# Optimization experiments

Measured on AMD Instinct MI355X. Metric: run time of the kernel, lower is better.

## Reference

```python
import jax, jax.numpy as jnp
import numpy as np

NEG_SLOPE = 0.2
EPS = 1e-16  # PyG softmax eps


def _gat_conv(x, src, dst, W, att_src, att_dst, bias, heads, out_ch):
    """PyG GATConv (eval mode, self-loops already appended, concat output)."""
    N = x.shape[0]
    xw = (x @ W).reshape(N, heads, out_ch)            # [N,H,C]
    a_src = jnp.sum(xw * att_src, axis=-1)            # [N,H]
    a_dst = jnp.sum(xw * att_dst, axis=-1)            # [N,H]
    e = jax.nn.leaky_relu(a_src[src] + a_dst[dst], NEG_SLOPE)  # [E,H]
    m = jax.ops.segment_max(e, dst, num_segments=N)   # [N,H] (self-loops -> no empty segs)
    e = jnp.exp(e - m[dst])
    denom = jax.ops.segment_sum(e, dst, num_segments=N)
    alpha = e / (denom[dst] + EPS)                    # [E,H]
    msg = xw[src] * alpha[:, :, None]                 # [E,H,C]
    out = jax.ops.segment_sum(msg, dst, num_segments=N)  # [N,H,C]
    return out.reshape(N, heads * out_ch) + bias


def setup_inputs() -> dict:
    key = jax.random.key(0)
    ks = jax.random.split(key, 12)
    N, E, F_in, H, C, NC = 20000, 320000, 512, 8, 64, 32
    x = jax.random.normal(ks[0], (N, F_in), dtype=jnp.float32)
    edge_index = jax.random.randint(ks[1], (2, E), 0, N, dtype=jnp.int64)
    g = lambda k, shape, fan: jax.random.normal(k, shape, dtype=jnp.float32) * (1.0 / np.sqrt(fan))
    return {
        "x": x,
        "edge_index": edge_index,
        "W1": g(ks[2], (F_in, H * C), F_in),
        "att_src1": g(ks[3], (H, C), C),
        "att_dst1": g(ks[4], (H, C), C),
        "b1": jnp.zeros((H * C,), dtype=jnp.float32),
        "W2": g(ks[5], (H * C, NC), H * C),
        "att_src2": g(ks[6], (1, NC), NC),
        "att_dst2": g(ks[7], (1, NC), NC),
        "b2": jnp.zeros((NC,), dtype=jnp.float32),
    }


def reference(x, edge_index, W1, att_src1, att_dst1, b1, W2, att_src2, att_dst2, b2):
    N = x.shape[0]
    H, C = att_src1.shape
    NC = att_src2.shape[1]
    # GATConv adds self-loops by default
    loops = jnp.arange(N, dtype=edge_index.dtype)
    src = jnp.concatenate([edge_index[0], loops])
    dst = jnp.concatenate([edge_index[1], loops])
    h = _gat_conv(x, src, dst, W1, att_src1, att_dst1, b1, H, C)
    h = jax.nn.elu(h)
    h = _gat_conv(h, src, dst, W2, att_src2, att_dst2, b2, 1, NC)
    return jax.nn.log_softmax(h, axis=1)
```

## Files before the change

kernel.cpp:

```cpp
#include <hip/hip_runtime.h>
#include <math.h>

#define NEG_SLOPE 0.2f
#define SM_EPS 1e-16f

typedef short short8 __attribute__((ext_vector_type(8)));
typedef float floatx4 __attribute__((ext_vector_type(4)));


__device__ inline unsigned short f2bf(float x) {
    unsigned int u = __float_as_uint(x);
    unsigned int r = (u + 0x7FFFu + ((u >> 16) & 1u)) >> 16;
    return (unsigned short)r;
}

__device__ inline float bf2f(unsigned short h) {
    return __uint_as_float(((unsigned int)h) << 16);
}

__device__ inline float bflo(unsigned int u) { return __uint_as_float(u << 16); }
__device__ inline float bfhi(unsigned int u) { return __uint_as_float(u & 0xFFFF0000u); }

__device__ __forceinline__ void gl_lds16(const unsigned short* g, unsigned short* l) {
    __builtin_amdgcn_global_load_lds(
        (const __attribute__((address_space(1))) unsigned int*)(g),
        (__attribute__((address_space(3))) unsigned int*)(l), 16, 0, 0);
}

__device__ inline void get_edge(const int* __restrict__ srcA, const int* __restrict__ dstA,
                                int e, int E, int& s, int& d) {
    if (e < E) { s = srcA[e]; d = dstA[e]; }
    else { s = e - E; d = e - E; }
}


__global__ __launch_bounds__(256) void k_prep(const float* __restrict__ x,
                                              unsigned short* __restrict__ xb,
                                              const float* __restrict__ W1,
                                              unsigned short* __restrict__ w1t,
                                              const float* __restrict__ W2,
                                              unsigned short* __restrict__ w2bt,
                                              const int* __restrict__ dstA,
                                              int E, int Ep,
                                              int* __restrict__ deg,
                                              int nblk_deg, int nblk_x) {
    __shared__ float tile[32][33];
    int bx = blockIdx.x;
    int t = threadIdx.x;
    if (bx < nblk_deg) {
        int e = bx * 256 + t;
        if (e < Ep) {
            int d = (e < E) ? dstA[e] : (e - E);
            atomicAdd(&deg[d], 1);
        }
    } else if (bx < nblk_deg + nblk_x) {
        int i = ((bx - nblk_deg) * 256 + t) * 4;
        float4 v = *(const float4*)(x + i);
        ushort4 o;
        o.x = f2bf(v.x); o.y = f2bf(v.y); o.z = f2bf(v.z); o.w = f2bf(v.w);
        *(ushort4*)(xb + i) = o;
    } else if (bx < nblk_deg + nblk_x + 256) {
        int b = bx - nblk_deg - nblk_x;
        int kb = (b & 15) * 32;
        int nb = (b >> 4) * 32;
        int tx = t & 31, ty = t >> 5;
        #pragma unroll
        for (int i = 0; i < 32; i += 8)
            tile[ty + i][tx] = W1[(size_t)(kb + ty + i) * 512 + nb + tx];
        __syncthreads();
        #pragma unroll
        for (int i = 0; i < 32; i += 8)
            w1t[(size_t)(nb + ty + i) * 512 + kb + tx] = f2bf(tile[tx][ty + i]);
    } else {
        int i = (bx - nblk_deg - nblk_x - 256) * 256 + t;
        int c = i >> 9, k = i & 511;
        w2bt[i] = f2bf(W2[k * 32 + c]);
    }
}


__global__ __launch_bounds__(256) void k_scan1(const int* __restrict__ deg, int* __restrict__ incl,
                                               int* __restrict__ part, int N) {
    __shared__ int sm[256];
    int t = threadIdx.x;
    int i = blockIdx.x * 256 + t;
    int v = (i < N) ? deg[i] : 0;
    sm[t] = v; __syncthreads();
    for (int o = 1; o < 256; o <<= 1) {
        int x = (t >= o) ? sm[t - o] : 0;
        __syncthreads();
        sm[t] += x;
        __syncthreads();
    }
    if (i < N) incl[i] = sm[t];
    if (t == 255) part[blockIdx.x] = sm[255];
}

__global__ __launch_bounds__(256) void k_scan3(const int* __restrict__ incl, const int* __restrict__ part,
                                               const int* __restrict__ deg, int* __restrict__ off,
                                               int* __restrict__ cursor, int N) {
    __shared__ int sm[256];
    int bx = blockIdx.x, t = threadIdx.x;
    int partial = 0;
    for (int i = t; i < bx; i += 256) partial += part[i];
    sm[t] = partial; __syncthreads();
    for (int o = 128; o > 0; o >>= 1) {
        if (t < o) sm[t] += sm[t + o];
        __syncthreads();
    }
    int base = sm[0];
    int i = bx * 256 + t;
    if (i >= N) return;
    int v = incl[i] + base;
    off[i + 1] = v;
    cursor[i] = v - deg[i];
    if (i == 0) off[0] = 0;
}

__global__ __launch_bounds__(256) void k_scatter(const int* __restrict__ srcA, const int* __restrict__ dstA,
                                                 int E, int Ep, int* __restrict__ cursor,
                                                 int* __restrict__ src_s) {
    int e = blockIdx.x * 256 + threadIdx.x;
    if (e >= Ep) return;
    int s, d; get_edge(srcA, dstA, e, E, s, d);
    int p = atomicAdd(&cursor[d], 1);
    src_s[p] = s;
}


__global__ __launch_bounds__(256) void k_gemm1_mfma(const unsigned short* __restrict__ A,
                                                    const unsigned short* __restrict__ Bt,
                                                    const float* __restrict__ att_s,
                                                    const float* __restrict__ att_d,
                                                    unsigned short* __restrict__ C,
                                                    float* __restrict__ a_sd,
                                                    float* __restrict__ a_dd, int M) {
    const int K = 512;
    __shared__ unsigned short As[128 * 32];
    __shared__ unsigned short Bs[128 * 32];
    int t = threadIdx.x;
    int lane = t & 63;
    int w = t >> 6;
    int row0 = blockIdx.x * 128;
    int col0 = blockIdx.y * 128;
    int wm = (w >> 1) * 64, wn = (w & 1) * 64;
    int l15 = lane & 15, q = lane >> 4;

    int mrow = t >> 2;
    int kk = (t & 3) * 8;
    unsigned short* ldsA0 = &As[w * 512];
    unsigned short* ldsA1 = &As[2048 + w * 512];
    unsigned short* ldsB0 = &Bs[w * 512];
    unsigned short* ldsB1 = &Bs[2048 + w * 512];

    floatx4 acc[4][4] = {};

    for (int k0 = 0; k0 < K; k0 += 32) {
        gl_lds16(A  + (size_t)(row0 + mrow) * K + k0 + kk,      ldsA0);
        gl_lds16(A  + (size_t)(row0 + 64 + mrow) * K + k0 + kk, ldsA1);
        gl_lds16(Bt + (size_t)(col0 + mrow) * K + k0 + kk,      ldsB0);
        gl_lds16(Bt + (size_t)(col0 + 64 + mrow) * K + k0 + kk, ldsB1);
        __syncthreads();
        short8 af[4], bfr[4];
        #pragma unroll
        for (int i = 0; i < 4; ++i)
            af[i] = *(const short8*)(&As[(wm + i * 16 + l15) * 32 + q * 8]);
        #pragma unroll
        for (int j = 0; j < 4; ++j)
            bfr[j] = *(const short8*)(&Bs[(wn + j * 16 + l15) * 32 + q * 8]);
        #pragma unroll
        for (int i = 0; i < 4; ++i)
            #pragma unroll
            for (int j = 0; j < 4; ++j)
                acc[i][j] = __builtin_amdgcn_mfma_f32_16x16x32_bf16(af[i], bfr[j], acc[i][j], 0, 0, 0);
        __syncthreads();
    }

    #pragma unroll
    for (int i = 0; i < 4; ++i) {
        #pragma unroll
        for (int p = 0; p < 4; ++p) {
            int r = row0 + wm + i * 16 + q * 4 + p;
            if (r < M) {
                #pragma unroll
                for (int j = 0; j < 4; ++j) {
                    int c = col0 + wn + j * 16 + l15;
                    C[(size_t)r * 512 + c] = f2bf(acc[i][j][p]);
                }
            }
        }
    }

    int hh = blockIdx.y * 2 + (w & 1);
    float asr[4], adr[4];
    #pragma unroll
    for (int j = 0; j < 4; ++j) {
        asr[j] = att_s[hh * 64 + j * 16 + l15];
        adr[j] = att_d[hh * 64 + j * 16 + l15];
    }
    #pragma unroll
    for (int i = 0; i < 4; ++i) {
        #pragma unroll
        for (int p = 0; p < 4; ++p) {
            float ds = 0.f, dd = 0.f;
            #pragma unroll
            for (int j = 0; j < 4; ++j) {
                ds = fmaf(acc[i][j][p], asr[j], ds);
                dd = fmaf(acc[i][j][p], adr[j], dd);
            }
            #pragma unroll
            for (int mk = 1; mk <= 8; mk <<= 1) {
                ds += __shfl_xor(ds, mk);
                dd += __shfl_xor(dd, mk);
            }
            int r = row0 + wm + i * 16 + q * 4 + p;
            if (l15 == 0 && r < M) {
                a_sd[(size_t)hh * M + r] = ds;
                a_dd[(size_t)hh * M + r] = dd;
            }
        }
    }
}


__global__ __launch_bounds__(256) void k_l1(const unsigned short* __restrict__ xw,
                                            const float* __restrict__ a_s,
                                            const float* __restrict__ a_d,
                                            const int* __restrict__ off,
                                            const int* __restrict__ src_s,
                                            const float* __restrict__ bias,
                                            unsigned short* __restrict__ hout, int N) {
    int wid = threadIdx.x >> 6, lane = threadIdx.x & 63;
    int h = blockIdx.x & 7;
    int n = (blockIdx.x >> 3) * 32 + wid * 8 + (lane >> 3);
    int li = lane & 7;
    if (n >= N) return;
    int p0 = off[n], p1 = off[n + 1];
    const float* ash = a_s + (size_t)h * N;
    float adv = a_d[(size_t)h * N + n];
    const size_t cbase = (size_t)h * 64 + (size_t)li * 8;

    float acc[8] = {};
    float s = 0.f;
    int p = p0;
    for (; p + 2 <= p1; p += 2) {
        int s0 = src_s[p];
        int s1 = src_s[p + 1];
        const uint4 u0 = *(const uint4*)(xw + (size_t)s0 * 512 + cbase);
        const uint4 u1 = *(const uint4*)(xw + (size_t)s1 * 512 + cbase);
        float e0 = ash[s0] + adv; e0 = e0 > 0.f ? e0 : NEG_SLOPE * e0;
        float e1 = ash[s1] + adv; e1 = e1 > 0.f ? e1 : NEG_SLOPE * e1;
        float w0 = __expf(e0);
        float w1 = __expf(e1);
        s += w0 + w1;
        acc[0] = fmaf(w0, bflo(u0.x), acc[0]); acc[1] = fmaf(w0, bfhi(u0.x), acc[1]);
        acc[2] = fmaf(w0, bflo(u0.y), acc[2]); acc[3] = fmaf(w0, bfhi(u0.y), acc[3]);
        acc[4] = fmaf(w0, bflo(u0.z), acc[4]); acc[5] = fmaf(w0, bfhi(u0.z), acc[5]);
        acc[6] = fmaf(w0, bflo(u0.w), acc[6]); acc[7] = fmaf(w0, bfhi(u0.w), acc[7]);
        acc[0] = fmaf(w1, bflo(u1.x), acc[0]); acc[1] = fmaf(w1, bfhi(u1.x), acc[1]);
        acc[2] = fmaf(w1, bflo(u1.y), acc[2]); acc[3] = fmaf(w1, bfhi(u1.y), acc[3]);
        acc[4] = fmaf(w1, bflo(u1.z), acc[4]); acc[5] = fmaf(w1, bfhi(u1.z), acc[5]);
        acc[6] = fmaf(w1, bflo(u1.w), acc[6]); acc[7] = fmaf(w1, bfhi(u1.w), acc[7]);
    }
    if (p < p1) {
        int s0 = src_s[p];
        const uint4 u0 = *(const uint4*)(xw + (size_t)s0 * 512 + cbase);
        float e0 = ash[s0] + adv; e0 = e0 > 0.f ? e0 : NEG_SLOPE * e0;
        float w0 = __expf(e0);
        s += w0;
        acc[0] = fmaf(w0, bflo(u0.x), acc[0]); acc[1] = fmaf(w0, bfhi(u0.x), acc[1]);
        acc[2] = fmaf(w0, bflo(u0.y), acc[2]); acc[3] = fmaf(w0, bfhi(u0.y), acc[3]);
        acc[4] = fmaf(w0, bflo(u0.z), acc[4]); acc[5] = fmaf(w0, bfhi(u0.z), acc[5]);
        acc[6] = fmaf(w0, bflo(u0.w), acc[6]); acc[7] = fmaf(w0, bfhi(u0.w), acc[7]);
    }

    float inv = 1.f / (s + SM_EPS);
    unsigned int ov[4];
    #pragma unroll
    for (int j = 0; j < 4; ++j) {
        float v0 = acc[2 * j] * inv     + bias[cbase + 2 * j];
        float v1 = acc[2 * j + 1] * inv + bias[cbase + 2 * j + 1];
        v0 = v0 > 0.f ? v0 : expm1f(v0);
        v1 = v1 > 0.f ? v1 : expm1f(v1);
        ov[j] = (unsigned int)f2bf(v0) | ((unsigned int)f2bf(v1) << 16);
    }
    *(uint4*)(hout + (size_t)n * 512 + cbase) = make_uint4(ov[0], ov[1], ov[2], ov[3]);
}


__global__ __launch_bounds__(256) void k_gemm2_mfma(const unsigned short* __restrict__ A,
                                                    const unsigned short* __restrict__ Bt,
                                                    const float* __restrict__ att_s,
                                                    const float* __restrict__ att_d,
                                                    unsigned short* __restrict__ O,
                                                    float* __restrict__ a_s, float* __restrict__ a_d,
                                                    int M) {
    const int K = 512;
    __shared__ unsigned short As[64 * 40];
    __shared__ unsigned short Bs[32 * 40];
    int t = threadIdx.x;
    int lane = t & 63;
    int w = t >> 6;
    int row0 = blockIdx.x * 64;
    int l15 = lane & 15, q = lane >> 4;

    floatx4 acc[2] = {};

    for (int k0 = 0; k0 < K; k0 += 32) {
        {
            int flat = t * 8;
            int m = flat >> 5, kk = flat & 31;
            uint4 va = make_uint4(0u, 0u, 0u, 0u);
            int gr = row0 + m;
            if (gr < M) va = *(const uint4*)(A + (size_t)gr * K + k0 + kk);
            *(uint4*)(&As[m * 40 + kk]) = va;
            if (t < 128) {
                int nn = t >> 2, kb = (t & 3) * 8;
                *(uint4*)(&Bs[nn * 40 + kb]) = *(const uint4*)(Bt + (size_t)nn * K + k0 + kb);
            }
        }
        __syncthreads();
        short8 af = *(const short8*)(&As[(w * 16 + l15) * 40 + q * 8]);
        short8 b0 = *(const short8*)(&Bs[(l15) * 40 + q * 8]);
        short8 b1 = *(const short8*)(&Bs[(16 + l15) * 40 + q * 8]);
        acc[0] = __builtin_amdgcn_mfma_f32_16x16x32_bf16(af, b0, acc[0], 0, 0, 0);
        acc[1] = __builtin_amdgcn_mfma_f32_16x16x32_bf16(af, b1, acc[1], 0, 0, 0);
        __syncthreads();
    }

    float as_lo = att_s[l15], as_hi = att_s[16 + l15];
    float ad_lo = att_d[l15], ad_hi = att_d[16 + l15];
    #pragma unroll
    for (int p = 0; p < 4; ++p) {
        int r = row0 + w * 16 + q * 4 + p;
        bool ok = r < M;
        float v0 = acc[0][p], v1 = acc[1][p];
        if (ok) {
            O[(size_t)r * 32 + l15]      = f2bf(v0);
            O[(size_t)r * 32 + 16 + l15] = f2bf(v1);
        }
        float ds = v0 * as_lo + v1 * as_hi;
        float dd = v0 * ad_lo + v1 * ad_hi;
        #pragma unroll
        for (int mk = 1; mk <= 8; mk <<= 1) {
            ds += __shfl_xor(ds, mk);
            dd += __shfl_xor(dd, mk);
        }
        if (ok && l15 == 0) { a_s[r] = ds; a_d[r] = dd; }
    }
}


__global__ __launch_bounds__(256) void k_l2(const unsigned short* __restrict__ hw2,
                                            const float* __restrict__ a_s,
                                            const float* __restrict__ a_d,
                                            const int* __restrict__ off,
                                            const int* __restrict__ src_s,
                                            const float* __restrict__ bias,
                                            float* __restrict__ outp, int N) {
    int wid = threadIdx.x >> 6, lane = threadIdx.x & 63;
    int n = blockIdx.x * 4 + wid;
    if (n >= N) return;
    int p0 = off[n], p1 = off[n + 1];
    float adv = a_d[n];
    int c = lane & 31, ep = lane >> 5;

    float acc = 0.f, s = 0.f;
    int p = p0;
    for (; p + 64 <= p1; p += 64) {
        int bsrc = src_s[p + lane];
        float e = a_s[bsrc] + adv;
        e = e > 0.f ? e : NEG_SLOPE * e;
        float w64 = __expf(e);
        #pragma unroll
        for (int j = 0; j < 64; j += 2) {
            int sj = __shfl(bsrc, j + ep);
            float wj = __shfl(w64, j + ep);
            s += wj;
            acc = fmaf(wj, bf2f(hw2[(size_t)sj * 32 + c]), acc);
        }
    }
    if (p < p1) {
        int nb = p1 - p;
        int bsrc = src_s[p + (lane < nb ? lane : 0)];
        float e = a_s[bsrc] + adv;
        e = e > 0.f ? e : NEG_SLOPE * e;
        float w64 = __expf(e);
        for (int j = 0; j < nb; j += 2) {
            int idx = j + ep;
            bool valid = idx < nb;
            int idc = valid ? idx : 0;
            int sj = __shfl(bsrc, idc);
            float wj = __shfl(w64, idc);
            if (valid) {
                s += wj;
                acc = fmaf(wj, bf2f(hw2[(size_t)sj * 32 + c]), acc);
            }
        }
    }
    acc += __shfl_xor(acc, 32);
    s   += __shfl_xor(s, 32);
    float v = acc / (s + SM_EPS) + bias[c];
    float mx = v;
    #pragma unroll
    for (int mk = 16; mk >= 1; mk >>= 1) mx = fmaxf(mx, __shfl_xor(mx, mk, 32));
    float ex = __expf(v - mx);
    float sum = ex;
    #pragma unroll
    for (int mk = 16; mk >= 1; mk >>= 1) sum += __shfl_xor(sum, mk, 32);
    if (lane < 32) outp[(size_t)n * 32 + c] = (v - mx) - __logf(sum);
}


extern "C" void kernel_launch(void* const* d_in, const int* in_sizes, int n_in,
                              void* d_out, int out_size, void* d_ws, size_t ws_size,
                              hipStream_t stream) {
    const float* x   = (const float*)d_in[0];
    const int*   ei  = (const int*)d_in[1];
    const float* W1  = (const float*)d_in[2];
    const float* as1 = (const float*)d_in[3];
    const float* ad1 = (const float*)d_in[4];
    const float* b1  = (const float*)d_in[5];
    const float* W2  = (const float*)d_in[6];
    const float* as2 = (const float*)d_in[7];
    const float* ad2 = (const float*)d_in[8];
    const float* b2  = (const float*)d_in[9];
    float* out = (float*)d_out;

    const int F = 512;
    const int N = in_sizes[0] / F;
    const int E = in_sizes[1] / 2;
    const int Ep = E + N;
    const int* srcA = ei;
    const int* dstA = ei + E;

    char* w = (char*)d_ws;
    auto alloc = [&](size_t b) -> void* {
        void* p = (void*)w;
        w += (b + 255) & ~(size_t)255;
        return p;
    };
    unsigned short* xbf  = (unsigned short*)alloc((size_t)N * 512 * 2);
    unsigned short* w1t  = (unsigned short*)alloc((size_t)512 * 512 * 2);
    unsigned short* w2bt = (unsigned short*)alloc((size_t)32 * 512 * 2);
    unsigned short* xw1  = (unsigned short*)alloc((size_t)N * 512 * 2);
    unsigned short* hbuf = (unsigned short*)alloc((size_t)N * 512 * 2);
    float* a_s1 = (float*)alloc((size_t)N * 8 * 4);
    float* a_d1 = (float*)alloc((size_t)N * 8 * 4);
    unsigned short* hw2 = (unsigned short*)alloc((size_t)N * 32 * 2);
    float* a_s2 = (float*)alloc((size_t)N * 4);
    float* a_d2 = (float*)alloc((size_t)N * 4);
    int* deg    = (int*)alloc((size_t)N * 4);
    int* incl   = (int*)alloc((size_t)N * 4);
    int* part   = (int*)alloc(256 * 4);
    int* off    = (int*)alloc((size_t)(N + 1) * 4);
    int* cursor = (int*)alloc((size_t)N * 4);
    int* src_s  = (int*)alloc((size_t)Ep * 4);

    int egrid = (Ep + 255) / 256;
    int sgrid = (N + 255) / 256;
    int ngrid4 = (N + 3) / 4;
    int nblk_x = (N * 512 / 4) / 256;
    int nblk_w2 = (32 * 512 + 255) / 256;

    hipMemsetAsync(deg, 0, (size_t)N * 4, stream);

    k_prep<<<egrid + nblk_x + 256 + nblk_w2, 256, 0, stream>>>(
        x, xbf, W1, w1t, W2, w2bt, dstA, E, Ep, deg, egrid, nblk_x);

    k_scan1<<<sgrid, 256, 0, stream>>>(deg, incl, part, N);
    k_scan3<<<sgrid, 256, 0, stream>>>(incl, part, deg, off, cursor, N);
    k_scatter<<<egrid, 256, 0, stream>>>(srcA, dstA, E, Ep, cursor, src_s);

    {
        dim3 g1((N + 127) / 128, 512 / 128);
        k_gemm1_mfma<<<g1, 256, 0, stream>>>(xbf, w1t, as1, ad1, xw1, a_s1, a_d1, N);
    }
    {
        int ngrid32 = (N + 31) / 32;
        k_l1<<<ngrid32 * 8, 256, 0, stream>>>(xw1, a_s1, a_d1, off, src_s, b1, hbuf, N);
    }

    k_gemm2_mfma<<<(N + 63) / 64, 256, 0, stream>>>(hbuf, w2bt, as2, ad2, hw2, a_s2, a_d2, N);
    k_l2<<<ngrid4, 256, 0, stream>>>(hw2, a_s2, a_d2, off, src_s, b2, out, N);
}
```

Baseline: 250.9 us.

## Sort nodes by degree bins to balance layer-1 aggregation work

Adds a 64-bin degree histogram during the scan, a bin prefix scan, and a permutation pass fused into the scatter kernel, so that the layer-1 aggregation kernel processes nodes grouped by similar in-degree. This is meant to cut divergence among the 8 nodes sharing a wavefront, whose loops run for different edge counts. It also swaps expm1f for __expf-1 in the ELU. The cost is an extra tiny kernel launch, global atomics on 64 bins, and output writes to permuted node rows, which scatters store locality.

```diff
diff --git a/kernel.cpp b/kernel.cpp
--- a/kernel.cpp
+++ b/kernel.cpp
@@ -80,12 +80,16 @@
 
 
 __global__ __launch_bounds__(256) void k_scan1(const int* __restrict__ deg, int* __restrict__ incl,
-                                               int* __restrict__ part, int N) {
+                                               int* __restrict__ part, int* __restrict__ bins, int N) {
     __shared__ int sm[256];
+    __shared__ int hist[64];
     int t = threadIdx.x;
+    if (t < 64) hist[t] = 0;
     int i = blockIdx.x * 256 + t;
     int v = (i < N) ? deg[i] : 0;
-    sm[t] = v; __syncthreads();
+    sm[t] = v;
+    __syncthreads();
+    if (i < N) atomicAdd(&hist[v < 63 ? v : 63], 1);
     for (int o = 1; o < 256; o <<= 1) {
         int x = (t >= o) ? sm[t - o] : 0;
         __syncthreads();
@@ -94,6 +98,15 @@
     }
     if (i < N) incl[i] = sm[t];
     if (t == 255) part[blockIdx.x] = sm[255];
+    __syncthreads();
+    if (t < 64 && hist[t]) atomicAdd(&bins[t], hist[t]);
+}
+
+__global__ void k_binscan(const int* __restrict__ bins, int* __restrict__ bincur) {
+    if (threadIdx.x == 0) {
+        int run = 0;
+        for (int i = 0; i < 64; ++i) { bincur[i] = run; run += bins[i]; }
+    }
 }
 
 __global__ __launch_bounds__(256) void k_scan3(const int* __restrict__ incl, const int* __restrict__ part,
@@ -119,12 +132,24 @@
 
 __global__ __launch_bounds__(256) void k_scatter(const int* __restrict__ srcA, const int* __restrict__ dstA,
                                                  int E, int Ep, int* __restrict__ cursor,
-                                                 int* __restrict__ src_s) {
-    int e = blockIdx.x * 256 + threadIdx.x;
-    if (e >= Ep) return;
-    int s, d; get_edge(srcA, dstA, e, E, s, d);
-    int p = atomicAdd(&cursor[d], 1);
-    src_s[p] = s;
+                                                 int* __restrict__ src_s,
+                                                 const int* __restrict__ deg,
+                                                 int* __restrict__ bincur, int* __restrict__ perm,
+                                                 int nblk_e, int N) {
+    int bx = blockIdx.x, t = threadIdx.x;
+    if (bx < nblk_e) {
+        int e = bx * 256 + t;
+        if (e >= Ep) return;
+        int s, d; get_edge(srcA, dstA, e, E, s, d);
+        int p = atomicAdd(&cursor[d], 1);
+        src_s[p] = s;
+    } else {
+        int i = (bx - nblk_e) * 256 + t;
+        if (i >= N) return;
+        int b = deg[i]; b = b < 63 ? b : 63;
+        int pos = atomicAdd(&bincur[b], 1);
+        perm[pos] = i;
+    }
 }
 
 
@@ -228,13 +253,15 @@
                                             const float* __restrict__ a_d,
                                             const int* __restrict__ off,
                                             const int* __restrict__ src_s,
+                                            const int* __restrict__ perm,
                                             const float* __restrict__ bias,
                                             unsigned short* __restrict__ hout, int N) {
     int wid = threadIdx.x >> 6, lane = threadIdx.x & 63;
     int h = blockIdx.x & 7;
-    int n = (blockIdx.x >> 3) * 32 + wid * 8 + (lane >> 3);
+    int slot = (blockIdx.x >> 3) * 32 + wid * 8 + (lane >> 3);
     int li = lane & 7;
-    if (n >= N) return;
+    if (slot >= N) return;
+    int n = perm[slot];
     int p0 = off[n], p1 = off[n + 1];
     const float* ash = a_s + (size_t)h * N;
     float adv = a_d[(size_t)h * N + n];
@@ -280,8 +307,8 @@
     for (int j = 0; j < 4; ++j) {
         float v0 = acc[2 * j] * inv     + bias[cbase + 2 * j];
         float v1 = acc[2 * j + 1] * inv + bias[cbase + 2 * j + 1];
-        v0 = v0 > 0.f ? v0 : expm1f(v0);
-        v1 = v1 > 0.f ? v1 : expm1f(v1);
+        v0 = v0 > 0.f ? v0 : __expf(v0) - 1.f;
+        v1 = v1 > 0.f ? v1 : __expf(v1) - 1.f;
         ov[j] = (unsigned int)f2bf(v0) | ((unsigned int)f2bf(v1) << 16);
     }
     *(uint4*)(hout + (size_t)n * 512 + cbase) = make_uint4(ov[0], ov[1], ov[2], ov[3]);
@@ -456,6 +483,9 @@
     int* off    = (int*)alloc((size_t)(N + 1) * 4);
     int* cursor = (int*)alloc((size_t)N * 4);
     int* src_s  = (int*)alloc((size_t)Ep * 4);
+    int* bins   = (int*)alloc(64 * 4);
+    int* bincur = (int*)alloc(64 * 4);
+    int* perm   = (int*)alloc((size_t)N * 4);
 
     int egrid = (Ep + 255) / 256;
     int sgrid = (N + 255) / 256;
@@ -464,13 +494,16 @@
     int nblk_w2 = (32 * 512 + 255) / 256;
 
     hipMemsetAsync(deg, 0, (size_t)N * 4, stream);
+    hipMemsetAsync(bins, 0, 64 * 4, stream);
 
     k_prep<<<egrid + nblk_x + 256 + nblk_w2, 256, 0, stream>>>(
         x, xbf, W1, w1t, W2, w2bt, dstA, E, Ep, deg, egrid, nblk_x);
 
-    k_scan1<<<sgrid, 256, 0, stream>>>(deg, incl, part, N);
+    k_scan1<<<sgrid, 256, 0, stream>>>(deg, incl, part, bins, N);
+    k_binscan<<<1, 64, 0, stream>>>(bins, bincur);
     k_scan3<<<sgrid, 256, 0, stream>>>(incl, part, deg, off, cursor, N);
-    k_scatter<<<egrid, 256, 0, stream>>>(srcA, dstA, E, Ep, cursor, src_s);
+    k_scatter<<<egrid + sgrid, 256, 0, stream>>>(srcA, dstA, E, Ep, cursor, src_s,
+                                                 deg, bincur, perm, egrid, N);
 
     {
         dim3 g1((N + 127) / 128, 512 / 128);
@@ -478,7 +511,7 @@
     }
     {
         int ngrid32 = (N + 31) / 32;
-        k_l1<<<ngrid32 * 8, 256, 0, stream>>>(xw1, a_s1, a_d1, off, src_s, b1, hbuf, N);
+        k_l1<<<ngrid32 * 8, 256, 0, stream>>>(xw1, a_s1, a_d1, off, src_s, perm, b1, hbuf, N);
     }
 
     k_gemm2_mfma<<<(N + 63) / 64, 256, 0, stream>>>(hbuf, w2bt, as2, ad2, hw2, a_s2, a_d2, N);
```

Result: slower. 305.2 us (+21.6%).
